# Kernel tuning notes

Measured on AMD Instinct MI355X. Metric: run time of the kernel, lower is better.

Reference implementation:

```python
import jax, jax.numpy as jnp
import numpy as np

T, D_MODEL = 2048, 6144
NH, NKV, HD = 48, 8, 128
THETA, CAP = 10000.0, 30.0


def setup_inputs() -> dict:
    key = jax.random.key(0)
    k1, k2, k3 = jax.random.split(key, 3)
    return {
        "positions": jnp.arange(T, dtype=jnp.int32),
        "hidden_states": jax.random.normal(k1, (T, D_MODEL), jnp.float32),
        "w_qkv": jax.random.normal(k2, (D_MODEL, (NH + 2 * NKV) * HD), jnp.float32) * 0.02,
        "w_o": jax.random.normal(k3, (NH * HD, D_MODEL), jnp.float32) * 0.02,
    }


def _rope_neox(positions, x):
    # x: [T, h, HD]; neox-style: rotate concatenated halves
    half = HD // 2
    inv_freq = 1.0 / (THETA ** (jnp.arange(0, HD, 2, dtype=jnp.float32) / HD))  # [half]
    freqs = positions.astype(jnp.float32)[:, None] * inv_freq  # [T, half]
    cos = jnp.cos(freqs)[:, None, :]  # [T,1,half]
    sin = jnp.sin(freqs)[:, None, :]
    x1, x2 = x[..., :half], x[..., half:]
    return jnp.concatenate([x1 * cos - x2 * sin, x2 * cos + x1 * sin], axis=-1)


def reference(positions, hidden_states, w_qkv, w_o):
    qkv = hidden_states @ w_qkv  # [T, (NH+2*NKV)*HD]
    q, k, v = jnp.split(qkv, [NH * HD, NH * HD + NKV * HD], axis=-1)
    q = q.reshape(T, NH, HD)
    k = k.reshape(T, NKV, HD)
    v = v.reshape(T, NKV, HD)
    q = _rope_neox(positions, q)
    k = _rope_neox(positions, k)
    # GQA: expand kv heads to query heads
    g = NH // NKV
    k = jnp.repeat(k, g, axis=1)  # [T, NH, HD]
    v = jnp.repeat(v, g, axis=1)
    scale = HD ** -0.5
    logits = jnp.einsum('thd,shd->hts', q, k) * scale  # [NH, T, T]
    logits = CAP * jnp.tanh(logits / CAP)  # tanh logit softcapping
    causal = positions[:, None] >= positions[None, :]  # [T, T]
    logits = jnp.where(causal[None, :, :], logits, -jnp.inf)
    probs = jax.nn.softmax(logits, axis=-1)
    out = jnp.einsum('hts,shd->thd', probs, v)  # [T, NH, HD]
    out = out.reshape(T, NH * HD)
    return out @ w_o
```

## Files before the change

kernel.cpp:

```cpp
#include <hip/hip_runtime.h>
#include <hip/hip_bf16.h>
#include <stdint.h>

#define TSEQ   2048
#define DMODEL 6144
#define NHEADS 48
#define NKVH   8
#define HDIM   128
#define QKVC   8192
#define GRP    6

typedef __attribute__((ext_vector_type(8))) short short8;
typedef __attribute__((ext_vector_type(4))) float f32x4;


__device__ __forceinline__ unsigned short f2b(float f) {
  union { float f; unsigned int u; } v; v.f = f;
  unsigned int u = v.u;
  unsigned int r = (u + 0x7FFFu + ((u >> 16) & 1u)) >> 16;
  return (unsigned short)r;
}

#if __has_builtin(__builtin_amdgcn_exp2f)
#define EXP2(x) __builtin_amdgcn_exp2f(x)
#else
#define EXP2(x) exp2f(x)
#endif
#if __has_builtin(__builtin_amdgcn_rcpf)
#define RCP(x) __builtin_amdgcn_rcpf(x)
#else
#define RCP(x) (1.0f / (x))
#endif

typedef const __attribute__((address_space(1))) void* as1_cvp;
typedef __attribute__((address_space(3))) void* as3_vp;

__device__ __forceinline__ void gload_lds16(const void* g, void* l) {
  __builtin_amdgcn_global_load_lds(
      (as1_cvp)(uintptr_t)g,
      (as3_vp)(unsigned int)(uintptr_t)l, 16, 0, 0);
}

#define LGKM0 do { asm volatile("s_waitcnt lgkmcnt(0)" ::: "memory"); \
                   __builtin_amdgcn_sched_barrier(0); } while (0)
#define VMC(n) do { asm volatile("s_waitcnt vmcnt(" #n ")" ::: "memory"); \
                    __builtin_amdgcn_sched_barrier(0); } while (0)
#define BARR  do { asm volatile("s_barrier" ::: "memory"); } while (0)


__global__ __launch_bounds__(256) void k_cvt(const float* __restrict__ in,
                                             unsigned short* __restrict__ outp, int n) {
  int i = (blockIdx.x * 256 + threadIdx.x) * 4;
  if (i + 3 < n) {
    float4 v = *(const float4*)(in + i);
    union { unsigned short s[4]; uint2 u; } o;
    o.s[0] = f2b(v.x); o.s[1] = f2b(v.y); o.s[2] = f2b(v.z); o.s[3] = f2b(v.w);
    *(uint2*)(outp + i) = o.u;
  }
}

__global__ __launch_bounds__(256) void k_tr(const float* __restrict__ in,
                                            unsigned short* __restrict__ out, int R, int C) {
  __shared__ unsigned short tile[64][65];
  const int tx = threadIdx.x & 63;
  const int ty = threadIdx.x >> 6;
  const int br = blockIdx.y * 64;
  const int bc = blockIdx.x * 64;
#pragma unroll
  for (int j = 0; j < 16; ++j) {
    int r = ty * 16 + j;
    tile[r][tx] = f2b(in[(size_t)(br + r) * C + bc + tx]);
  }
  __syncthreads();
#pragma unroll
  for (int j = 0; j < 16; ++j) {
    int r = ty * 16 + j;
    out[(size_t)(bc + r) * R + br + tx] = tile[tx][r];
  }
}

__global__ void k_trig(const int* __restrict__ pos, float* __restrict__ cs,
                       float* __restrict__ sn) {
  int t = blockIdx.x, i = threadIdx.x;
  float p = (float)pos[t];
  float inv = EXP2(-(float)(2 * i) * (1.0f / 128.0f) * 13.287712379549449f);
  float f = p * inv;
  cs[t * 64 + i] = cosf(f);
  sn[t * 64 + i] = sinf(f);
}


#define READ_A(mh) do { \
  _Pragma("unroll") for (int m = 0; m < 4; ++m) \
  _Pragma("unroll") for (int ks = 0; ks < 2; ++ks) \
    a[m][ks] = *(const short8*)(LA + (wm * 128 + (mh) * 64 + m * 16 + lr) * 128 \
                                + ((ks * 64 + lkb) ^ lsw)); } while (0)

#define READ_B(nh) do { \
  _Pragma("unroll") for (int n2 = 0; n2 < 2; ++n2) \
  _Pragma("unroll") for (int ks = 0; ks < 2; ++ks) \
    b[n2][ks] = *(const short8*)(LB + (wn * 64 + (nh) * 32 + n2 * 16 + lr) * 128 \
                                 + ((ks * 64 + lkb) ^ lsw)); } while (0)

#define CLUSTER(mh, nh) do { \
  __builtin_amdgcn_s_setprio(1); \
  _Pragma("unroll") for (int m = 0; m < 4; ++m) \
  _Pragma("unroll") for (int n2 = 0; n2 < 2; ++n2) \
  _Pragma("unroll") for (int ks = 0; ks < 2; ++ks) \
    acc[(mh) * 4 + m][(nh) * 2 + n2] = __builtin_amdgcn_mfma_f32_16x16x32_bf16( \
        a[m][ks], b[n2][ks], acc[(mh) * 4 + m][(nh) * 2 + n2], 0, 0, 0); \
  __builtin_amdgcn_s_setprio(0); } while (0)

#define STAGE_A(kt, bb) do { \
  _Pragma("unroll") for (int i = 0; i < 4; ++i) \
    gload_lds16(Asrc + (size_t)(kt) * 64 + (size_t)i * 64 * K, \
                lds + (bb) * 65536 + F + i * 8192); } while (0)

#define STAGE_B(kt, bb) do { \
  _Pragma("unroll") for (int i = 0; i < 4; ++i) \
    gload_lds16(Bsrc + (size_t)(kt) * 64 + (size_t)i * 64 * K, \
                lds + (bb) * 65536 + 32768 + F + i * 8192); } while (0)

__global__ __launch_bounds__(512, 2) void k_gemm8(const unsigned short* __restrict__ A,
                                                  const unsigned short* __restrict__ Bt,
                                                  float* __restrict__ C,
                                                  int M, int N, int K) {
  extern __shared__ __align__(16) unsigned char lds[];
  const int tid  = threadIdx.x;
  const int lane = tid & 63;
  const int wave = tid >> 6;
  const int wm = wave >> 2;
  const int wn = wave & 3;
  const int lr  = lane & 15;
  const int lkb = (lane >> 4) * 16;
  const int li4 = (lane >> 4) * 4;
  const int lsw = (lane & 7) << 4;

  const int mt = M >> 8;
  const int nt = N >> 8;
  const int Cx = nt >> 3;
  const int lin = blockIdx.x;
  const int xcd = lin & 7;
  const int r   = lin >> 3;
  const int m0  = (r % mt) << 8;
  const int n0  = (xcd * Cx + r / mt) << 8;

  const int F   = tid * 16;
  const int r0  = F >> 7;
  const int cbs = (F & 127) ^ ((r0 & 7) << 4);
  const unsigned short* Asrc = A  + (size_t)(m0 + r0) * K + (cbs >> 1);
  const unsigned short* Bsrc = Bt + (size_t)(n0 + r0) * K + (cbs >> 1);

  const int NT = K >> 6;

  f32x4 acc[8][4];
#pragma unroll
  for (int i = 0; i < 8; ++i)
#pragma unroll
    for (int j = 0; j < 4; ++j) acc[i][j] = (f32x4){0.f, 0.f, 0.f, 0.f};

  STAGE_A(0, 0);
  STAGE_B(0, 0);
  STAGE_A(1, 1);
  VMC(4);
  BARR;

  for (int t = 0; t < NT; ++t) {
    const int cur = t & 1;
    const unsigned char* LA = lds + cur * 65536;
    const unsigned char* LB = LA + 32768;
    short8 a[4][2], b[2][2];

    READ_A(0);
    READ_B(0);
    if (t + 1 < NT) STAGE_B(t + 1, cur ^ 1);
    LGKM0;
    CLUSTER(0, 0);
    BARR;

    READ_B(1);
    LGKM0;
    CLUSTER(0, 1);
    BARR;

    READ_A(1);
    READ_B(0);
    LGKM0;
    CLUSTER(1, 0);
    BARR;

    READ_B(1);
    if (t + 2 < NT) STAGE_A(t + 2, cur);
    LGKM0;
    CLUSTER(1, 1);
    if (t + 2 < NT) { VMC(4); } else { VMC(0); }
    BARR;
  }

#pragma unroll
  for (int mh = 0; mh < 2; ++mh)
#pragma unroll
    for (int m = 0; m < 4; ++m)
#pragma unroll
      for (int nh = 0; nh < 2; ++nh)
#pragma unroll
        for (int n2 = 0; n2 < 2; ++n2)
#pragma unroll
          for (int i = 0; i < 4; ++i) {
            int row = m0 + wm * 128 + mh * 64 + m * 16 + li4 + i;
            int col = n0 + wn * 64 + nh * 32 + n2 * 16 + lr;
            C[(size_t)row * N + col] = acc[mh * 4 + m][nh * 2 + n2][i];
          }
}


__global__ __launch_bounds__(256) void k_rope(const float* __restrict__ qkv,
                                              const float* __restrict__ cs,
                                              const float* __restrict__ sn,
                                              unsigned short* __restrict__ Q,
                                              unsigned short* __restrict__ K,
                                              unsigned short* __restrict__ Vt) {
  const int t = blockIdx.x;
  const int tid = threadIdx.x;
  const float* row = qkv + (size_t)t * QKVC;
  const float* c = cs + t * 64;
  const float* s = sn + t * 64;
  for (int p = tid; p < NHEADS * 64; p += 256) {
    int h = p >> 6, i = p & 63;
    float x1 = row[h * 128 + i], x2 = row[h * 128 + 64 + i];
    float cc = c[i], ss = s[i];
    size_t base = ((size_t)h * TSEQ + t) * HDIM;
    Q[base + i]      = f2b(x1 * cc - x2 * ss);
    Q[base + 64 + i] = f2b(x2 * cc + x1 * ss);
  }
  for (int p = tid; p < NKVH * 64; p += 256) {
    int h = p >> 6, i = p & 63;
    float x1 = row[DMODEL + h * 128 + i], x2 = row[DMODEL + h * 128 + 64 + i];
    float cc = c[i], ss = s[i];
    size_t base = ((size_t)h * TSEQ + t) * HDIM;
    K[base + i]      = f2b(x1 * cc - x2 * ss);
    K[base + 64 + i] = f2b(x2 * cc + x1 * ss);
  }
  for (int p = tid; p < NKVH * HDIM; p += 256) {
    int h = p >> 7, d = p & 127;
    Vt[((size_t)h * HDIM + d) * TSEQ + t] = f2b(row[DMODEL + NKVH * HDIM + h * 128 + d]);
  }
}


__global__ __launch_bounds__(256, 3) void k_attn2(const unsigned short* __restrict__ Q,
                                                  const unsigned short* __restrict__ K,
                                                  const unsigned short* __restrict__ V,
                                                  unsigned short* __restrict__ O) {
  __shared__ __align__(16) unsigned char KsB[16384];
  __shared__ __align__(16) unsigned char VsB[16384];
  __shared__ __align__(16) unsigned char PsB[4][2048];

  const int lin = blockIdx.x;
  const int g   = lin & 7;
  const int rr  = lin >> 3;
  const int hg  = rr % 6;
  const int pr  = rr / 6;
  const int h   = g * 6 + hg;
  const int tid = threadIdx.x, wave = tid >> 6, lane = tid & 63;
  const int lr = lane & 15, lk = (lane >> 4) * 8, li4 = (lane >> 4) * 4;
  const unsigned short* Qh = Q + (size_t)h * (TSEQ * HDIM);
  const unsigned char*  Kb = (const unsigned char*)(K + (size_t)g * (TSEQ * HDIM));
  const unsigned char*  Vb = (const unsigned char*)(V + (size_t)g * (TSEQ * HDIM));
  unsigned char* Pw = PsB[wave];

  for (int half = 0; half < 2; ++half) {
    const int j  = half ? (31 - pr) : pr;
    const int t0 = j * 64 + wave * 16;
    const int nst = j + 1;

    short8 qf[4];
#pragma unroll
    for (int ks = 0; ks < 4; ++ks)
      qf[ks] = *(const short8*)(Qh + (size_t)(t0 + lr) * HDIM + ks * 32 + lk);

    f32x4 oacc[8];
#pragma unroll
    for (int n = 0; n < 8; ++n) oacc[n] = (f32x4){0.f, 0.f, 0.f, 0.f};
    float rs4[4] = {0.f, 0.f, 0.f, 0.f};

    for (int st = 0; st < nst; ++st) {
      const int s0 = st * 64;
#pragma unroll
      for (int c = 0; c < 4; ++c) {
        const int FF = tid * 16 + c * 4096;
        const int krow = FF >> 8;
        const int kcol = (FF & 255) ^ ((krow & 7) << 4);
        gload_lds16(Kb + (size_t)(s0 + krow) * 256 + kcol, KsB + FF);
        const int vrow = FF >> 7;
        const int vcol = (FF & 127) ^ ((vrow & 7) << 4);
        gload_lds16(Vb + (size_t)vrow * (TSEQ * 2) + (size_t)s0 * 2 + vcol, VsB + FF);
      }
      __syncthreads();

      f32x4 sacc[4];
#pragma unroll
      for (int n = 0; n < 4; ++n) sacc[n] = (f32x4){0.f, 0.f, 0.f, 0.f};
#pragma unroll
      for (int ks = 0; ks < 4; ++ks) {
        short8 kf[4];
#pragma unroll
        for (int n = 0; n < 4; ++n) {
          const int row = n * 16 + lr;
          kf[n] = *(const short8*)(KsB + row * 256 + ((ks * 64 + lk * 2) ^ ((row & 7) << 4)));
        }
#pragma unroll
        for (int n = 0; n < 4; ++n)
          sacc[n] = __builtin_amdgcn_mfma_f32_16x16x32_bf16(qf[ks], kf[n], sacc[n], 0, 0, 0);
      }

      const bool lastst = (st == nst - 1);
#pragma unroll
      for (int n = 0; n < 4; ++n)
#pragma unroll
        for (int i = 0; i < 4; ++i) {
          float sv = sacc[n][i] * 0.08838834764831845f;
          float e = EXP2(sv * 0.09617966939259757f);
          float p = EXP2(-86.5617024533378f * RCP(e + 1.0f));
          if (lastst && (s0 + n * 16 + lr > t0 + li4 + i)) p = 0.f;
          rs4[i] += p;
          const int prow = li4 + i;
          *(unsigned short*)(Pw + prow * 128 +
              (((n * 16 + lr) * 2) ^ ((prow & 7) << 4))) = f2b(p);
        }

#pragma unroll
      for (int ks2 = 0; ks2 < 2; ++ks2) {
        short8 pf = *(const short8*)(Pw + lr * 128 +
                         (((ks2 * 32 + lk) * 2) ^ ((lr & 7) << 4)));
        short8 vf[8];
#pragma unroll
        for (int n = 0; n < 8; ++n) {
          const int row = n * 16 + lr;
          vf[n] = *(const short8*)(VsB + row * 128 + ((ks2 * 64 + lk * 2) ^ ((row & 7) << 4)));
        }
#pragma unroll
        for (int n = 0; n < 8; ++n)
          oacc[n] = __builtin_amdgcn_mfma_f32_16x16x32_bf16(pf, vf[n], oacc[n], 0, 0, 0);
      }
      __syncthreads();
    }

    float inv4[4];
#pragma unroll
    for (int i = 0; i < 4; ++i) {
      float v = rs4[i];
      v += __shfl_xor(v, 1, 64);
      v += __shfl_xor(v, 2, 64);
      v += __shfl_xor(v, 4, 64);
      v += __shfl_xor(v, 8, 64);
      inv4[i] = RCP(v);
    }
#pragma unroll
    for (int n = 0; n < 8; ++n)
#pragma unroll
      for (int i = 0; i < 4; ++i)
        O[(size_t)(t0 + li4 + i) * DMODEL + h * HDIM + n * 16 + lr] =
            f2b(oacc[n][i] * inv4[i]);
  }
}


extern "C" void kernel_launch(void* const* d_in, const int* in_sizes, int n_in,
                              void* d_out, int out_size, void* d_ws, size_t ws_size,
                              hipStream_t stream) {
  const int*   pos  = (const int*)d_in[0];
  const float* hid  = (const float*)d_in[1];
  const float* wqkv = (const float*)d_in[2];
  const float* wo   = (const float*)d_in[3];
  float* out = (float*)d_out;
  char* ws = (char*)d_ws;

  const size_t O_XB   = 0;
  const size_t O_WQT  = 25165824;
  const size_t O_WOT  = 125829120;
  const size_t O_QKV  = 201326592;
  const size_t O_TRIG = 268435456;

  unsigned short* Xb  = (unsigned short*)(ws + O_XB);
  unsigned short* Wqt = (unsigned short*)(ws + O_WQT);
  unsigned short* Wot = (unsigned short*)(ws + O_WOT);
  float* QKV = (float*)(ws + O_QKV);
  float* CS  = (float*)(ws + O_TRIG);
  float* SN  = CS + TSEQ * 64;
  unsigned short* Qr = Wqt;
  unsigned short* Kr = Wqt + (size_t)NHEADS * TSEQ * HDIM;
  unsigned short* Vt = Kr + (size_t)NKVH * TSEQ * HDIM;
  unsigned short* AO = Xb;

  hipFuncSetAttribute((const void*)k_gemm8,
                      hipFuncAttributeMaxDynamicSharedMemorySize, 131072);

  k_cvt<<<(TSEQ * DMODEL) / (256 * 4), 256, 0, stream>>>(hid, Xb, TSEQ * DMODEL);
  k_tr<<<dim3(QKVC / 64, DMODEL / 64), 256, 0, stream>>>(wqkv, Wqt, DMODEL, QKVC);
  k_tr<<<dim3(DMODEL / 64, DMODEL / 64), 256, 0, stream>>>(wo, Wot, DMODEL, DMODEL);
  k_trig<<<TSEQ, 64, 0, stream>>>(pos, CS, SN);

  k_gemm8<<<(TSEQ / 256) * (QKVC / 256), 512, 131072, stream>>>(Xb, Wqt, QKV,
                                                                TSEQ, QKVC, DMODEL);
  k_rope<<<TSEQ, 256, 0, stream>>>(QKV, CS, SN, Qr, Kr, Vt);
  k_attn2<<<768, 256, 0, stream>>>(Qr, Kr, Vt, AO);
  k_gemm8<<<(TSEQ / 256) * (DMODEL / 256), 512, 131072, stream>>>(AO, Wot, out,
                                                                  TSEQ, DMODEL, DMODEL);
}
```

Measured before the change: 571.5 us.

## Vectorize conversion, transpose and RoPE kernels; reuse B fragments in GEMM

Widens the fp32-to-bf16 conversion to 8 elements per thread and rewrites the transpose kernel to read float4 and write packed 4-element rows, with a batched z dimension. RoPE now handles Q and K heads in one vectorized loop, and the V transpose moves into a separate batched transpose launch instead of scattered 2-byte stores. In the GEMM main loop, both B fragment halves are held in registers so the second A half reuses them rather than re-reading LDS. This costs more VGPRs in the GEMM and adds one extra kernel launch.

```diff
diff --git a/kernel.cpp b/kernel.cpp
--- a/kernel.cpp
+++ b/kernel.cpp
@@ -50,32 +50,46 @@
 
 __global__ __launch_bounds__(256) void k_cvt(const float* __restrict__ in,
                                              unsigned short* __restrict__ outp, int n) {
-  int i = (blockIdx.x * 256 + threadIdx.x) * 4;
-  if (i + 3 < n) {
-    float4 v = *(const float4*)(in + i);
-    union { unsigned short s[4]; uint2 u; } o;
-    o.s[0] = f2b(v.x); o.s[1] = f2b(v.y); o.s[2] = f2b(v.z); o.s[3] = f2b(v.w);
-    *(uint2*)(outp + i) = o.u;
-  }
-}
-
-__global__ __launch_bounds__(256) void k_tr(const float* __restrict__ in,
-                                            unsigned short* __restrict__ out, int R, int C) {
-  __shared__ unsigned short tile[64][65];
-  const int tx = threadIdx.x & 63;
-  const int ty = threadIdx.x >> 6;
+  int i = (blockIdx.x * 256 + threadIdx.x) * 8;
+  if (i + 7 < n) {
+    float4 va = *(const float4*)(in + i);
+    float4 vb = *(const float4*)(in + i + 4);
+    union { unsigned short s[8]; uint4 u; } o;
+    o.s[0] = f2b(va.x); o.s[1] = f2b(va.y); o.s[2] = f2b(va.z); o.s[3] = f2b(va.w);
+    o.s[4] = f2b(vb.x); o.s[5] = f2b(vb.y); o.s[6] = f2b(vb.z); o.s[7] = f2b(vb.w);
+    *(uint4*)(outp + i) = o.u;
+  }
+}
+
+__global__ __launch_bounds__(256) void k_tr2(const float* __restrict__ in, long istr, long zin,
+                                             unsigned short* __restrict__ out, long ostr, long zout) {
+  __shared__ unsigned short tile[64][68];
+  const int tid = threadIdx.x;
   const int br = blockIdx.y * 64;
   const int bc = blockIdx.x * 64;
-#pragma unroll
-  for (int j = 0; j < 16; ++j) {
-    int r = ty * 16 + j;
-    tile[r][tx] = f2b(in[(size_t)(br + r) * C + bc + tx]);
+  in  += (size_t)blockIdx.z * zin;
+  out += (size_t)blockIdx.z * zout;
+  const int row = tid >> 4;
+  const int c4  = (tid & 15) * 4;
+#pragma unroll
+  for (int p = 0; p < 4; ++p) {
+    const int r = p * 16 + row;
+    float4 v = *(const float4*)(in + (size_t)(br + r) * istr + bc + c4);
+    tile[r][c4 + 0] = f2b(v.x);
+    tile[r][c4 + 1] = f2b(v.y);
+    tile[r][c4 + 2] = f2b(v.z);
+    tile[r][c4 + 3] = f2b(v.w);
   }
   __syncthreads();
 #pragma unroll
-  for (int j = 0; j < 16; ++j) {
-    int r = ty * 16 + j;
-    out[(size_t)(bc + r) * R + br + tx] = tile[tx][r];
+  for (int p = 0; p < 4; ++p) {
+    const int r = p * 16 + row;
+    union { unsigned short s[4]; uint2 u; } o;
+    o.s[0] = tile[c4 + 0][r];
+    o.s[1] = tile[c4 + 1][r];
+    o.s[2] = tile[c4 + 2][r];
+    o.s[3] = tile[c4 + 3][r];
+    *(uint2*)(out + (size_t)(bc + r) * ostr + br + c4) = o.u;
   }
 }
 
@@ -96,19 +110,19 @@
     a[m][ks] = *(const short8*)(LA + (wm * 128 + (mh) * 64 + m * 16 + lr) * 128 \
                                 + ((ks * 64 + lkb) ^ lsw)); } while (0)
 
-#define READ_B(nh) do { \
+#define READ_B(nh, bb) do { \
   _Pragma("unroll") for (int n2 = 0; n2 < 2; ++n2) \
   _Pragma("unroll") for (int ks = 0; ks < 2; ++ks) \
-    b[n2][ks] = *(const short8*)(LB + (wn * 64 + (nh) * 32 + n2 * 16 + lr) * 128 \
-                                 + ((ks * 64 + lkb) ^ lsw)); } while (0)
-
-#define CLUSTER(mh, nh) do { \
+    bb[n2][ks] = *(const short8*)(LB + (wn * 64 + (nh) * 32 + n2 * 16 + lr) * 128 \
+                                  + ((ks * 64 + lkb) ^ lsw)); } while (0)
+
+#define CLUSTER(mh, nh, bb) do { \
   __builtin_amdgcn_s_setprio(1); \
   _Pragma("unroll") for (int m = 0; m < 4; ++m) \
   _Pragma("unroll") for (int n2 = 0; n2 < 2; ++n2) \
   _Pragma("unroll") for (int ks = 0; ks < 2; ++ks) \
     acc[(mh) * 4 + m][(nh) * 2 + n2] = __builtin_amdgcn_mfma_f32_16x16x32_bf16( \
-        a[m][ks], b[n2][ks], acc[(mh) * 4 + m][(nh) * 2 + n2], 0, 0, 0); \
+        a[m][ks], bb[n2][ks], acc[(mh) * 4 + m][(nh) * 2 + n2], 0, 0, 0); \
   __builtin_amdgcn_s_setprio(0); } while (0)
 
 #define STAGE_A(kt, bb) do { \
@@ -169,30 +183,27 @@
     const int cur = t & 1;
     const unsigned char* LA = lds + cur * 65536;
     const unsigned char* LB = LA + 32768;
-    short8 a[4][2], b[2][2];
+    short8 a[4][2], b0[2][2], b1[2][2];
 
     READ_A(0);
-    READ_B(0);
+    READ_B(0, b0);
     if (t + 1 < NT) STAGE_B(t + 1, cur ^ 1);
     LGKM0;
-    CLUSTER(0, 0);
+    CLUSTER(0, 0, b0);
     BARR;
 
-    READ_B(1);
+    READ_B(1, b1);
     LGKM0;
-    CLUSTER(0, 1);
+    CLUSTER(0, 1, b1);
     BARR;
 
     READ_A(1);
-    READ_B(0);
     LGKM0;
-    CLUSTER(1, 0);
+    CLUSTER(1, 0, b0);
     BARR;
 
-    READ_B(1);
     if (t + 2 < NT) STAGE_A(t + 2, cur);
-    LGKM0;
-    CLUSTER(1, 1);
+    CLUSTER(1, 1, b1);
     if (t + 2 < NT) { VMC(4); } else { VMC(0); }
     BARR;
   }
@@ -218,32 +229,33 @@
                                               const float* __restrict__ cs,
                                               const float* __restrict__ sn,
                                               unsigned short* __restrict__ Q,
-                                              unsigned short* __restrict__ K,
-                                              unsigned short* __restrict__ Vt) {
+                                              unsigned short* __restrict__ K) {
   const int t = blockIdx.x;
   const int tid = threadIdx.x;
   const float* row = qkv + (size_t)t * QKVC;
   const float* c = cs + t * 64;
   const float* s = sn + t * 64;
-  for (int p = tid; p < NHEADS * 64; p += 256) {
-    int h = p >> 6, i = p & 63;
-    float x1 = row[h * 128 + i], x2 = row[h * 128 + 64 + i];
-    float cc = c[i], ss = s[i];
-    size_t base = ((size_t)h * TSEQ + t) * HDIM;
-    Q[base + i]      = f2b(x1 * cc - x2 * ss);
-    Q[base + 64 + i] = f2b(x2 * cc + x1 * ss);
-  }
-  for (int p = tid; p < NKVH * 64; p += 256) {
-    int h = p >> 6, i = p & 63;
-    float x1 = row[DMODEL + h * 128 + i], x2 = row[DMODEL + h * 128 + 64 + i];
-    float cc = c[i], ss = s[i];
-    size_t base = ((size_t)h * TSEQ + t) * HDIM;
-    K[base + i]      = f2b(x1 * cc - x2 * ss);
-    K[base + 64 + i] = f2b(x2 * cc + x1 * ss);
-  }
-  for (int p = tid; p < NKVH * HDIM; p += 256) {
-    int h = p >> 7, d = p & 127;
-    Vt[((size_t)h * HDIM + d) * TSEQ + t] = f2b(row[DMODEL + NKVH * HDIM + h * 128 + d]);
+  for (int p = tid; p < 56 * 16; p += 256) {
+    const int h = p >> 4, q4 = (p & 15) * 4;
+    const float* src = row + h * 128;
+    float4 x1 = *(const float4*)(src + q4);
+    float4 x2 = *(const float4*)(src + 64 + q4);
+    float4 cc = *(const float4*)(c + q4);
+    float4 ss = *(const float4*)(s + q4);
+    unsigned short* dst = (h < NHEADS)
+        ? Q + ((size_t)h * TSEQ + t) * HDIM
+        : K + ((size_t)(h - NHEADS) * TSEQ + t) * HDIM;
+    union { unsigned short sh[4]; uint2 u; } o1, o2;
+    o1.sh[0] = f2b(x1.x * cc.x - x2.x * ss.x);
+    o1.sh[1] = f2b(x1.y * cc.y - x2.y * ss.y);
+    o1.sh[2] = f2b(x1.z * cc.z - x2.z * ss.z);
+    o1.sh[3] = f2b(x1.w * cc.w - x2.w * ss.w);
+    o2.sh[0] = f2b(x2.x * cc.x + x1.x * ss.x);
+    o2.sh[1] = f2b(x2.y * cc.y + x1.y * ss.y);
+    o2.sh[2] = f2b(x2.z * cc.z + x1.z * ss.z);
+    o2.sh[3] = f2b(x2.w * cc.w + x1.w * ss.w);
+    *(uint2*)(dst + q4) = o1.u;
+    *(uint2*)(dst + 64 + q4) = o2.u;
   }
 }
 
@@ -396,14 +408,17 @@
   hipFuncSetAttribute((const void*)k_gemm8,
                       hipFuncAttributeMaxDynamicSharedMemorySize, 131072);
 
-  k_cvt<<<(TSEQ * DMODEL) / (256 * 4), 256, 0, stream>>>(hid, Xb, TSEQ * DMODEL);
-  k_tr<<<dim3(QKVC / 64, DMODEL / 64), 256, 0, stream>>>(wqkv, Wqt, DMODEL, QKVC);
-  k_tr<<<dim3(DMODEL / 64, DMODEL / 64), 256, 0, stream>>>(wo, Wot, DMODEL, DMODEL);
+  k_cvt<<<(TSEQ * DMODEL) / (256 * 8), 256, 0, stream>>>(hid, Xb, TSEQ * DMODEL);
+  k_tr2<<<dim3(QKVC / 64, DMODEL / 64, 1), 256, 0, stream>>>(wqkv, QKVC, 0, Wqt, DMODEL, 0);
+  k_tr2<<<dim3(DMODEL / 64, DMODEL / 64, 1), 256, 0, stream>>>(wo, DMODEL, 0, Wot, DMODEL, 0);
   k_trig<<<TSEQ, 64, 0, stream>>>(pos, CS, SN);
 
   k_gemm8<<<(TSEQ / 256) * (QKVC / 256), 512, 131072, stream>>>(Xb, Wqt, QKV,
                                                                 TSEQ, QKVC, DMODEL);
-  k_rope<<<TSEQ, 256, 0, stream>>>(QKV, CS, SN, Qr, Kr, Vt);
+  k_rope<<<TSEQ, 256, 0, stream>>>(QKV, CS, SN, Qr, Kr);
+  k_tr2<<<dim3(HDIM / 64, TSEQ / 64, NKVH), 256, 0, stream>>>(
+      QKV + (size_t)(DMODEL + NKVH * HDIM), QKVC, HDIM,
+      Vt, TSEQ, (size_t)HDIM * TSEQ);
   k_attn2<<<768, 256, 0, stream>>>(Qr, Kr, Vt, AO);
   k_gemm8<<<(TSEQ / 256) * (DMODEL / 256), 512, 131072, stream>>>(AO, Wot, out,
                                                                   TSEQ, DMODEL, DMODEL);
```

New measurement: 554.7 us. -2.9%, faster.
